# Optimization experiments

Hardware: AMD Instinct MI355X
Metric: run time of the kernel (lower is better)

## Reference

```python
import jax, jax.numpy as jnp
import numpy as np

N_ENT = 50000
N_REL = 16
N_EDGE = 1000000
D = 64


def setup_inputs() -> dict:
    key = jax.random.key(0)
    ks = jax.random.split(key, 20)
    inp = {
        'ent_embed': jax.random.normal(ks[0], (N_ENT, D), jnp.float32) * 0.1,
        'rel_embed': jax.random.normal(ks[1], (N_REL, D), jnp.float32) * 0.1,
        'W_R': jax.random.normal(ks[2], (N_REL, D, D), jnp.float32) * 0.1,
        'W1_0': jax.random.normal(ks[3], (64, 64), jnp.float32) * 0.1,
        'b1_0': jax.random.normal(ks[4], (64,), jnp.float32) * 0.1,
        'W2_0': jax.random.normal(ks[5], (64, 64), jnp.float32) * 0.1,
        'b2_0': jax.random.normal(ks[6], (64,), jnp.float32) * 0.1,
        'W1_1': jax.random.normal(ks[7], (64, 32), jnp.float32) * 0.1,
        'b1_1': jax.random.normal(ks[8], (32,), jnp.float32) * 0.1,
        'W2_1': jax.random.normal(ks[9], (64, 32), jnp.float32) * 0.1,
        'b2_1': jax.random.normal(ks[10], (32,), jnp.float32) * 0.1,
        'W1_2': jax.random.normal(ks[11], (32, 16), jnp.float32) * 0.1,
        'b1_2': jax.random.normal(ks[12], (16,), jnp.float32) * 0.1,
        'W2_2': jax.random.normal(ks[13], (32, 16), jnp.float32) * 0.1,
        'b2_2': jax.random.normal(ks[14], (16,), jnp.float32) * 0.1,
        'src': jax.random.randint(ks[15], (N_EDGE,), 0, N_ENT, jnp.int32),
        'dst': jax.random.randint(ks[16], (N_EDGE,), 0, N_ENT, jnp.int32),
        'etype': jax.random.randint(ks[17], (N_EDGE,), 0, N_REL, jnp.int32),
    }
    return inp


def _l2_normalize(x, eps=1e-12):
    # matches torch F.normalize(p=2, dim=1)
    n = jnp.sqrt(jnp.sum(x * x, axis=1, keepdims=True))
    return x / jnp.maximum(n, eps)


def _kgat_forward(ent_embed, rel_embed, W_R, layer_params, src, dst, etype):
    N = ent_embed.shape[0]
    # --- compute_attention: per-relation TransR projection of all entities ---
    # equivalent to per-edge ent[src] @ W_R[type] without materializing [E, D, D]
    proj = jnp.einsum('nd,rde->rne', ent_embed, W_R)          # [R, N, D]
    r_mul_t = proj[etype, src]                                # [E, D] (tail = src)
    r_mul_h = proj[etype, dst]                                # [E, D] (head = dst)
    att = jnp.sum(r_mul_t * jnp.tanh(r_mul_h + rel_embed[etype]), axis=-1)  # [E]
    # edge softmax grouped by destination node
    m = jax.ops.segment_max(att, dst, num_segments=N)         # [N]
    e = jnp.exp(att - m[dst])
    s = jax.ops.segment_sum(e, dst, num_segments=N)           # [N]
    a = e / s[dst]                                            # [E]

    # --- cf_embedding: bi-interaction aggregator layers ---
    h = ent_embed
    all_embed = [h]
    for (W1, b1, W2, b2) in layer_params:
        msg = a[:, None] * h[src]                             # [E, d_in]
        N_h = jax.ops.segment_sum(msg, dst, num_segments=N)   # [N, d_in]
        out = (jax.nn.leaky_relu((h + N_h) @ W1 + b1, 0.01)
               + jax.nn.leaky_relu((h * N_h) @ W2 + b2, 0.01))
        h = out
        all_embed.append(_l2_normalize(out))
    return jnp.concatenate(all_embed, axis=1)                 # [N, 64+64+32+16=176]


def reference(ent_embed, rel_embed, W_R,
              W1_0, b1_0, W2_0, b2_0,
              W1_1, b1_1, W2_1, b2_1,
              W1_2, b1_2, W2_2, b2_2,
              src, dst, etype):
    layer_params = [(W1_0, b1_0, W2_0, b2_0),
                    (W1_1, b1_1, W2_1, b2_1),
                    (W1_2, b1_2, W2_2, b2_2)]
    return _kgat_forward(ent_embed, rel_embed, W_R, layer_params, src, dst, etype)
```

## Files before the change

kernel.cpp:

```cpp
#include <hip/hip_runtime.h>
#include <hip/hip_bf16.h>
#include <cmath>

#define N_ENT  50000
#define N_RELS 16
#define N_EDGE 1000000
#define DIM    64
#define OUT_STRIDE 176

typedef float f32x4 __attribute__((ext_vector_type(4)));
typedef short s16x8 __attribute__((ext_vector_type(8)));

__device__ inline void bf16x8_unpack(uint4 u, float* f) {
    f[0] = __uint_as_float((u.x & 0xffffu) << 16);
    f[1] = __uint_as_float(u.x & 0xffff0000u);
    f[2] = __uint_as_float((u.y & 0xffffu) << 16);
    f[3] = __uint_as_float(u.y & 0xffff0000u);
    f[4] = __uint_as_float((u.z & 0xffffu) << 16);
    f[5] = __uint_as_float(u.z & 0xffff0000u);
    f[6] = __uint_as_float((u.w & 0xffffu) << 16);
    f[7] = __uint_as_float(u.w & 0xffff0000u);
}

__device__ inline ushort f2bf(float x) {
    __hip_bfloat16 b = __float2bfloat16(x);
    return *(ushort*)&b;
}

__device__ inline uint cvt_pk_bf16(float lo, float hi) {
    uint r;
    asm("v_cvt_pk_bf16_f32 %0, %1, %2" : "=v"(r) : "v"(lo), "v"(hi));
    return r;
}

__device__ __host__ inline int pcol(int p) {
    int qp = (p >> 3) & 7;
    int k  = p & 7;
    return 16 * (k >> 1) + 2 * qp + (k & 1);
}

__global__ __launch_bounds__(256) void prep_convert_kernel(
        const float* __restrict__ ent,
        ushort* __restrict__ ent_pi,
        float* __restrict__ out) {
    int i = blockIdx.x * blockDim.x + threadIdx.x;
    if (i < N_ENT * DIM) {
        float v = ent[i];
        ushort b = f2bf(v);
        int n = i >> 6, c = i & 63;
        int pos = ((c & 15) >> 1) * 8 + ((c >> 4) << 1) + (c & 1);
        ent_pi[(size_t)n * 64 + pos] = b;
        out[(size_t)n * OUT_STRIDE + c] = v;
    }
}

__global__ __launch_bounds__(256) void scan1_kernel(
        const int* __restrict__ counts, int* __restrict__ excl,
        int* __restrict__ bsum, int n) {
    __shared__ int sh[256];
    int t = threadIdx.x;
    int i = blockIdx.x * 256 + t;
    int c = (i < n) ? counts[i] : 0;
    sh[t] = c;
    __syncthreads();
    for (int off = 1; off < 256; off <<= 1) {
        int v = (t >= off) ? sh[t - off] : 0;
        __syncthreads();
        sh[t] += v;
        __syncthreads();
    }
    if (i < n) excl[i] = sh[t] - c;
    if (t == 255) bsum[blockIdx.x] = sh[255];
}

__global__ __launch_bounds__(256) void scan2_kernel(
        const int* __restrict__ bsum, int* __restrict__ boff,
        int* __restrict__ row_ptr, int nb, int n) {
    __shared__ int sh[256];
    int t = threadIdx.x;
    int v = (t < nb) ? bsum[t] : 0;
    sh[t] = v;
    __syncthreads();
    for (int off = 1; off < 256; off <<= 1) {
        int x = (t >= off) ? sh[t - off] : 0;
        __syncthreads();
        sh[t] += x;
        __syncthreads();
    }
    if (t < nb) boff[t] = sh[t] - v;
    if (t == nb - 1) row_ptr[n] = sh[t];
}

__global__ __launch_bounds__(256) void scan3_pos_kernel(
        const int* __restrict__ excl, const int* __restrict__ boff,
        int* __restrict__ row_ptr,
        const int* __restrict__ src, const int* __restrict__ dst,
        const int* __restrict__ etype, const int* __restrict__ off,
        unsigned long long* __restrict__ einfo) {
    int i = blockIdx.x * blockDim.x + threadIdx.x;
    if (i < N_ENT) row_ptr[i] = excl[i] + boff[i >> 8];
    if (i < N_EDGE) {
        int d = dst[i];
        int pos = excl[d] + boff[d >> 8] + off[i];
        unsigned long long info =
              (unsigned long long)(unsigned)src[i]
            | ((unsigned long long)(unsigned)d << 16)
            | ((unsigned long long)(unsigned)etype[i] << 32);
        einfo[pos] = info;
    }
}

__device__ __forceinline__ void gz_body(
        int r, int wid, int nw, int lane,
        const ushort* __restrict__ ent_pi,
        const float*  __restrict__ W_R,
        const float*  __restrict__ rel,
        ushort* __restrict__ Z,
        float* __restrict__ myLds) {
    int m = lane & 15;
    int q = lane >> 4;

    const float* Wr = W_R + (size_t)r * DIM * DIM;
    s16x8 b1[4][2], b2[4][2];
#pragma unroll
    for (int c = 0; c < 4; ++c)
#pragma unroll
        for (int ch = 0; ch < 2; ++ch)
#pragma unroll
            for (int j = 0; j < 8; ++j) {
                b1[c][ch][j] = (short)f2bf(Wr[pcol(ch * 32 + q * 8 + j) * DIM + c * 16 + m]);
                b2[c][ch][j] = (short)f2bf(Wr[(c * 16 + m) * DIM + ch * 32 + q * 8 + j]);
            }
    float relv[4];
#pragma unroll
    for (int c = 0; c < 4; ++c) relv[c] = rel[r * DIM + c * 16 + m];

    int par = m & 1;
    const int ntiles = N_ENT / 16;

    for (int t = wid; t < ntiles; t += nw) {
        int row0 = t * 16;
        const s16x8* arow = (const s16x8*)(ent_pi + (size_t)(row0 + m) * DIM);
        s16x8 a0 = arow[q];
        s16x8 a1 = arow[4 + q];
        f32x4 acc[4];
#pragma unroll
        for (int c = 0; c < 4; ++c) acc[c] = (f32x4){0.f, 0.f, 0.f, 0.f};
#pragma unroll
        for (int c = 0; c < 4; ++c) {
            acc[c] = __builtin_amdgcn_mfma_f32_16x16x32_bf16(a0, b1[c][0], acc[c], 0, 0, 0);
            acc[c] = __builtin_amdgcn_mfma_f32_16x16x32_bf16(a1, b1[c][1], acc[c], 0, 0, 0);
        }
#pragma unroll
        for (int c = 0; c < 4; ++c)
#pragma unroll
            for (int i = 0; i < 4; ++i) {
                float x = acc[c][i] + relv[c];
                float e2 = __expf(2.f * x);
                float g = 1.f - 2.f * __builtin_amdgcn_rcpf(e2 + 1.f);
                myLds[(q * 4 + i) * 68 + c * 16 + m] = g;
            }
        union { uint u[4]; s16x8 v; } a2u[2];
#pragma unroll
        for (int ch = 0; ch < 2; ++ch) {
            const f32x4* gp = (const f32x4*)(myLds + m * 68 + ch * 32 + q * 8);
            f32x4 g0 = gp[0];
            f32x4 g1 = gp[1];
            a2u[ch].u[0] = cvt_pk_bf16(g0[0], g0[1]);
            a2u[ch].u[1] = cvt_pk_bf16(g0[2], g0[3]);
            a2u[ch].u[2] = cvt_pk_bf16(g1[0], g1[1]);
            a2u[ch].u[3] = cvt_pk_bf16(g1[2], g1[3]);
        }

        f32x4 zacc[4];
#pragma unroll
        for (int c = 0; c < 4; ++c) zacc[c] = (f32x4){0.f, 0.f, 0.f, 0.f};
#pragma unroll
        for (int c = 0; c < 4; ++c) {
            zacc[c] = __builtin_amdgcn_mfma_f32_16x16x32_bf16(a2u[0].v, b2[c][0], zacc[c], 0, 0, 0);
            zacc[c] = __builtin_amdgcn_mfma_f32_16x16x32_bf16(a2u[1].v, b2[c][1], zacc[c], 0, 0, 0);
        }

        int rowA = row0 + 4 * q + (par ? 2 : 0);
        ushort* zb = Z + ((size_t)r * N_ENT + rowA) * 64 + (m >> 1) * 8;
#pragma unroll
        for (int rep = 0; rep < 2; ++rep) {
            uint4 Wv;
#pragma unroll
            for (int c = 0; c < 4; ++c) {
                float send = par ? zacc[c][rep] : zacc[c][2 + rep];
                float own  = par ? zacc[c][2 + rep] : zacc[c][rep];
                float oth  = __shfl_xor(send, 1, 64);
                float lo = par ? oth : own;
                float hi = par ? own : oth;
                ((uint*)&Wv)[c] = cvt_pk_bf16(lo, hi);
            }
            *(uint4*)(zb + rep * 64) = Wv;
        }
    }
}

#define HIST_LANES 131072

__global__ __launch_bounds__(256, 4) void gz_hist_kernel(
        const ushort* __restrict__ ent_pi,
        const float*  __restrict__ W_R,
        const float*  __restrict__ rel,
        ushort* __restrict__ Z,
        const int* __restrict__ dst,
        int* __restrict__ counts,
        int* __restrict__ off) {
    __shared__ __align__(16) float lds[3][16 * 68 + 16];
    int lane = threadIdx.x & 63;
    int wv   = threadIdx.x >> 6;

    if (wv == 3) {
        int lane_gid = blockIdx.x * 64 + lane;
        int d[8]; bool v[8]; int o[8];
#pragma unroll
        for (int k = 0; k < 8; ++k) {
            int i = lane_gid + k * HIST_LANES;
            v[k] = (i < N_EDGE);
            d[k] = v[k] ? dst[i] : 0;
        }
#pragma unroll
        for (int k = 0; k < 8; ++k)
            if (v[k]) o[k] = atomicAdd(&counts[d[k]], 1);
#pragma unroll
        for (int k = 0; k < 8; ++k)
            if (v[k]) off[lane_gid + k * HIST_LANES] = o[k];
        return;
    }

    int r   = blockIdx.x >> 7;
    int xb  = blockIdx.x & 127;
    int wid = xb * 3 + wv;
    gz_body(r, wid, 384, lane, ent_pi, W_R, rel, Z, lds[wv]);
}

__global__ __launch_bounds__(256) void att_dot_kernel(
        const ushort* __restrict__ ent_pi,
        const ushort* __restrict__ Z,
        const unsigned long long* __restrict__ einfo,
        uint2* __restrict__ es_csr,
        int n_edge) {
    int tid  = blockIdx.x * blockDim.x + threadIdx.x;
    int lane = threadIdx.x & 63;
    int sub  = lane >> 3;
    int q    = lane & 7;
    int base = (tid >> 6) * 32;
    if (base >= n_edge) return;

    int e[4];
    unsigned long long inf[4];
#pragma unroll
    for (int k = 0; k < 4; ++k) {
        e[k] = base + k * 8 + sub;
        inf[k] = einfo[e[k]];
    }

    int s[4], p_r[4], p_d[4];
#pragma unroll
    for (int k = 0; k < 4; ++k) {
        s[k]   = (int)(inf[k] & 0xffffu);
        p_d[k] = (int)((inf[k] >> 16) & 0xffffu);
        p_r[k] = (int)((inf[k] >> 32) & 0xfu);
    }

    uint4 uz[4], ue[4];
#pragma unroll
    for (int k = 0; k < 4; ++k) {
        uz[k] = *(const uint4*)(Z + ((size_t)p_r[k] * N_ENT + p_d[k]) * DIM + q * 8);
        ue[k] = *(const uint4*)(ent_pi + (size_t)s[k] * DIM + q * 8);
    }

    float pr[4];
#pragma unroll
    for (int k = 0; k < 4; ++k) {
        float zv[8], ev[8];
        bf16x8_unpack(uz[k], zv);
        bf16x8_unpack(ue[k], ev);
        float p = 0.f;
#pragma unroll
        for (int j = 0; j < 8; ++j) p = fmaf(ev[j], zv[j], p);
        pr[k] = p;
    }
#pragma unroll
    for (int k = 0; k < 4; ++k) {
        pr[k] += __shfl_xor(pr[k], 1, 64);
        pr[k] += __shfl_xor(pr[k], 2, 64);
        pr[k] += __shfl_xor(pr[k], 4, 64);
    }

    if (q == 0) {
#pragma unroll
        for (int k = 0; k < 4; ++k)
            es_csr[e[k]] = make_uint2(__float_as_uint(pr[k]), (unsigned)s[k]);
    }
}

__global__ __launch_bounds__(256) void agg64s_kernel(
        const ushort* __restrict__ tab,
        const uint2* __restrict__ es_csr,
        const int* __restrict__ row_ptr,
        float2* __restrict__ stats,
        float* __restrict__ N_h, int n_node) {
    int wid  = (blockIdx.x * blockDim.x + threadIdx.x) >> 6;
    int lane = threadIdx.x & 63;
    if (wid >= n_node) return;
    int q   = lane & 7;
    int sub = lane >> 3;

    int start = row_ptr[wid], end = row_ptr[wid + 1];

    float mx = -INFINITY;
    for (int i = start + lane; i < end; i += 64)
        mx = fmaxf(mx, __uint_as_float(es_csr[i].x));
#pragma unroll
    for (int o = 32; o > 0; o >>= 1)
        mx = fmaxf(mx, __shfl_xor(mx, o, 64));
    float ssum = 0.f;
    for (int i = start + lane; i < end; i += 64)
        ssum += __expf(__uint_as_float(es_csr[i].x) - mx);
#pragma unroll
    for (int o = 32; o > 0; o >>= 1)
        ssum += __shfl_xor(ssum, o, 64);
    float inv = (end > start) ? (1.0f / ssum) : 0.f;
    if (lane == 0) stats[wid] = make_float2(mx, inv);

    float acc[8];
#pragma unroll
    for (int j = 0; j < 8; ++j) acc[j] = 0.f;

    for (int p = start + sub; p < end; p += 8) {
        uint2 es = es_csr[p];
        float av = __expf(__uint_as_float(es.x) - mx);
        int   si = (int)es.y;
        uint4 u  = *(const uint4*)(tab + (size_t)si * 64 + q * 8);
        float g[8];
        bf16x8_unpack(u, g);
#pragma unroll
        for (int j = 0; j < 8; ++j) acc[j] = fmaf(av, g[j], acc[j]);
    }
#pragma unroll
    for (int mask = 8; mask < 64; mask <<= 1)
#pragma unroll
        for (int j = 0; j < 8; ++j)
            acc[j] += __shfl_xor(acc[j], mask, 64);

    if (sub == 0) {
        float* dstp = N_h + (size_t)wid * 64 + q * 8;
        *(float4*)(dstp)     = (float4){acc[0] * inv, acc[1] * inv, acc[2] * inv, acc[3] * inv};
        *(float4*)(dstp + 4) = (float4){acc[4] * inv, acc[5] * inv, acc[6] * inv, acc[7] * inv};
    }
}

__global__ __launch_bounds__(256) void agg64_kernel(
        const ushort* __restrict__ tab,
        const uint2* __restrict__ es_csr,
        const int* __restrict__ row_ptr,
        const float2* __restrict__ stats,
        float* __restrict__ N_h, int n_node) {
    int wid  = (blockIdx.x * blockDim.x + threadIdx.x) >> 6;
    int lane = threadIdx.x & 63;
    if (wid >= n_node) return;
    int q   = lane & 7;
    int sub = lane >> 3;

    int start = row_ptr[wid], end = row_ptr[wid + 1];
    float2 st = stats[wid];
    float mx = st.x, inv = st.y;
    float acc[8];
#pragma unroll
    for (int j = 0; j < 8; ++j) acc[j] = 0.f;

    for (int p = start + sub; p < end; p += 8) {
        uint2 es = es_csr[p];
        float av = __expf(__uint_as_float(es.x) - mx);
        int   si = (int)es.y;
        uint4 u  = *(const uint4*)(tab + (size_t)si * 64 + q * 8);
        float g[8];
        bf16x8_unpack(u, g);
#pragma unroll
        for (int j = 0; j < 8; ++j) acc[j] = fmaf(av, g[j], acc[j]);
    }
#pragma unroll
    for (int mask = 8; mask < 64; mask <<= 1)
#pragma unroll
        for (int j = 0; j < 8; ++j)
            acc[j] += __shfl_xor(acc[j], mask, 64);

    if (sub == 0) {
        float* dstp = N_h + (size_t)wid * 64 + q * 8;
        *(float4*)(dstp)     = (float4){acc[0] * inv, acc[1] * inv, acc[2] * inv, acc[3] * inv};
        *(float4*)(dstp + 4) = (float4){acc[4] * inv, acc[5] * inv, acc[6] * inv, acc[7] * inv};
    }
}

__global__ __launch_bounds__(256) void agg32_kernel(
        const ushort* __restrict__ tab,
        const uint2* __restrict__ es_csr,
        const int* __restrict__ row_ptr,
        const float2* __restrict__ stats,
        float* __restrict__ N_h, int n_node) {
    int wid  = (blockIdx.x * blockDim.x + threadIdx.x) >> 6;
    int lane = threadIdx.x & 63;
    if (wid >= n_node) return;
    int q   = lane & 3;
    int sub = lane >> 2;

    int start = row_ptr[wid], end = row_ptr[wid + 1];
    float2 st = stats[wid];
    float mx = st.x, inv = st.y;
    float acc[8];
#pragma unroll
    for (int j = 0; j < 8; ++j) acc[j] = 0.f;

    for (int p = start + sub; p < end; p += 16) {
        uint2 es = es_csr[p];
        float av = __expf(__uint_as_float(es.x) - mx);
        int   si = (int)es.y;
        uint4 u  = *(const uint4*)(tab + (size_t)si * 32 + q * 8);
        float g[8];
        bf16x8_unpack(u, g);
#pragma unroll
        for (int j = 0; j < 8; ++j) acc[j] = fmaf(av, g[j], acc[j]);
    }
#pragma unroll
    for (int mask = 4; mask < 64; mask <<= 1)
#pragma unroll
        for (int j = 0; j < 8; ++j)
            acc[j] += __shfl_xor(acc[j], mask, 64);

    if (sub == 0) {
        float* dstp = N_h + (size_t)wid * 32 + q * 8;
        *(float4*)(dstp)     = (float4){acc[0] * inv, acc[1] * inv, acc[2] * inv, acc[3] * inv};
        *(float4*)(dstp + 4) = (float4){acc[4] * inv, acc[5] * inv, acc[6] * inv, acc[7] * inv};
    }
}

template <int D_IN, int D_OUT, bool PERM>
__global__ __launch_bounds__(256) void mlp_mfma_kernel(
        const ushort* __restrict__ h,
        const float* __restrict__ N_h,
        const float* __restrict__ W1, const float* __restrict__ b1,
        const float* __restrict__ W2, const float* __restrict__ b2,
        ushort* __restrict__ ho,
        float* __restrict__ out_buf, int out_col) {
    constexpr int CH = D_IN / 32;
    constexpr int CT = D_OUT / 16;

    int lane = threadIdx.x & 63;
    int m    = lane & 15;
    int q    = lane >> 4;
    int wid  = blockIdx.x * (blockDim.x >> 6) + (threadIdx.x >> 6);
    int nw   = gridDim.x * (blockDim.x >> 6);

    s16x8 bu[CT][CH], bv[CT][CH];
#pragma unroll
    for (int c = 0; c < CT; ++c)
#pragma unroll
        for (int ch = 0; ch < CH; ++ch)
#pragma unroll
            for (int j = 0; j < 8; ++j) {
                int p = ch * 32 + q * 8 + j;
                int k = PERM ? pcol(p) : p;
                bu[c][ch][j] = (short)f2bf(W1[k * D_OUT + c * 16 + m]);
                bv[c][ch][j] = (short)f2bf(W2[k * D_OUT + c * 16 + m]);
            }

    const int ntiles = N_ENT / 16;
    for (int t = wid; t < ntiles; t += nw) {
        int row0 = t * 16;
        s16x8 au[CH], av[CH];
#pragma unroll
        for (int ch = 0; ch < CH; ++ch) {
            uint4 hu = *(const uint4*)(h + (size_t)(row0 + m) * D_IN + ch * 32 + q * 8);
            float hv8[8];
            bf16x8_unpack(hu, hv8);
            const float4* np = (const float4*)(N_h + (size_t)(row0 + m) * D_IN + ch * 32 + q * 8);
            float4 na = np[0], nb = np[1];
            float nv[8] = {na.x, na.y, na.z, na.w, nb.x, nb.y, nb.z, nb.w};
#pragma unroll
            for (int j = 0; j < 8; ++j) {
                au[ch][j] = (short)f2bf(hv8[j] + nv[j]);
                av[ch][j] = (short)f2bf(hv8[j] * nv[j]);
            }
        }

        f32x4 accu[CT], accv[CT];
#pragma unroll
        for (int c = 0; c < CT; ++c) {
            accu[c] = (f32x4){0.f, 0.f, 0.f, 0.f};
            accv[c] = (f32x4){0.f, 0.f, 0.f, 0.f};
        }
#pragma unroll
        for (int c = 0; c < CT; ++c)
#pragma unroll
            for (int ch = 0; ch < CH; ++ch) {
                accu[c] = __builtin_amdgcn_mfma_f32_16x16x32_bf16(au[ch], bu[c][ch], accu[c], 0, 0, 0);
                accv[c] = __builtin_amdgcn_mfma_f32_16x16x32_bf16(av[ch], bv[c][ch], accv[c], 0, 0, 0);
            }

        float res[CT][4];
        float sq[4] = {0.f, 0.f, 0.f, 0.f};
#pragma unroll
        for (int c = 0; c < CT; ++c) {
            float bb1 = b1[c * 16 + m];
            float bb2 = b2[c * 16 + m];
#pragma unroll
            for (int i = 0; i < 4; ++i) {
                float o1 = accu[c][i] + bb1;
                float o2 = accv[c][i] + bb2;
                float r1 = (o1 >= 0.f) ? o1 : 0.01f * o1;
                float r2 = (o2 >= 0.f) ? o2 : 0.01f * o2;
                float rr = r1 + r2;
                res[c][i] = rr;
                sq[i] = fmaf(rr, rr, sq[i]);
            }
        }
#pragma unroll
        for (int mask = 1; mask < 16; mask <<= 1)
#pragma unroll
            for (int i = 0; i < 4; ++i)
                sq[i] += __shfl_xor(sq[i], mask, 64);

#pragma unroll
        for (int i = 0; i < 4; ++i) {
            int row = row0 + q * 4 + i;
            float inv = 1.f / fmaxf(sqrtf(sq[i]), 1e-12f);
#pragma unroll
            for (int c = 0; c < CT; ++c) {
                int col = c * 16 + m;
                out_buf[(size_t)row * OUT_STRIDE + out_col + col] = res[c][i] * inv;
                if (ho) ho[(size_t)row * D_OUT + col] = f2bf(res[c][i]);
            }
        }
    }
}

extern "C" void kernel_launch(void* const* d_in, const int* in_sizes, int n_in,
                              void* d_out, int out_size, void* d_ws, size_t ws_size,
                              hipStream_t stream) {
    const float* ent  = (const float*)d_in[0];
    const float* rel  = (const float*)d_in[1];
    const float* W_R  = (const float*)d_in[2];
    const float* W1_0 = (const float*)d_in[3];
    const float* b1_0 = (const float*)d_in[4];
    const float* W2_0 = (const float*)d_in[5];
    const float* b2_0 = (const float*)d_in[6];
    const float* W1_1 = (const float*)d_in[7];
    const float* b1_1 = (const float*)d_in[8];
    const float* W2_1 = (const float*)d_in[9];
    const float* b2_1 = (const float*)d_in[10];
    const float* W1_2 = (const float*)d_in[11];
    const float* b1_2 = (const float*)d_in[12];
    const float* W2_2 = (const float*)d_in[13];
    const float* b2_2 = (const float*)d_in[14];
    const int*   src   = (const int*)d_in[15];
    const int*   dst   = (const int*)d_in[16];
    const int*   etype = (const int*)d_in[17];
    float* out = (float*)d_out;

    char* w = (char*)d_ws;
    uint2*  es_csr  = (uint2*)w;  w += (size_t)N_EDGE * 8;
    int*    counts  = (int*)w;    w += (size_t)(N_ENT + 64) * 4;
    int*    row_ptr = (int*)w;    w += (size_t)(N_ENT + 64) * 4;
    float2* stats   = (float2*)w; w += (size_t)(N_ENT + 64) * 8;
    int*    excl    = (int*)w;    w += (size_t)(N_ENT + 64) * 4;
    int*    bsum    = (int*)w;    w += 256 * 4;
    int*    boff    = (int*)w;    w += 256 * 4;
    ushort* ent_pi  = (ushort*)w; w += (size_t)N_ENT * 64 * 2;
    ushort* h1      = (ushort*)w; w += (size_t)N_ENT * 64 * 2;
    ushort* h2      = (ushort*)w; w += (size_t)N_ENT * 32 * 2;
    float*  N_h     = (float*)w;  w += (size_t)N_ENT * 64 * 4;
    ushort* Z       = (ushort*)w;
    (void)ws_size;

    int* off = (int*)es_csr;
    unsigned long long* einfo = (unsigned long long*)N_h;

    hipMemsetAsync(counts, 0, (size_t)N_ENT * 4, stream);

    const int nb = (N_ENT + 255) / 256;

    prep_convert_kernel<<<(N_ENT * DIM + 255) / 256, 256, 0, stream>>>(
        ent, ent_pi, out);

    gz_hist_kernel<<<2048, 256, 0, stream>>>(
        ent_pi, W_R, rel, Z, dst, counts, off);

    scan1_kernel<<<nb, 256, 0, stream>>>(counts, excl, bsum, N_ENT);
    scan2_kernel<<<1, 256, 0, stream>>>(bsum, boff, row_ptr, nb, N_ENT);
    scan3_pos_kernel<<<(N_EDGE + 255) / 256, 256, 0, stream>>>(
        excl, boff, row_ptr, src, dst, etype, off, einfo);

    att_dot_kernel<<<((N_EDGE + 31) / 32 * 64 + 255) / 256, 256, 0, stream>>>(
        ent_pi, Z, einfo, es_csr, N_EDGE);

    const int aggGrid = (N_ENT + 3) / 4;
    const int mlpGrid = 782;

    agg64s_kernel<<<aggGrid, 256, 0, stream>>>(ent_pi, es_csr, row_ptr, stats, N_h, N_ENT);
    mlp_mfma_kernel<64, 64, true><<<mlpGrid, 256, 0, stream>>>(
        ent_pi, N_h, W1_0, b1_0, W2_0, b2_0, h1, out, 64);

    agg64_kernel<<<aggGrid, 256, 0, stream>>>(h1, es_csr, row_ptr, stats, N_h, N_ENT);
    mlp_mfma_kernel<64, 32, false><<<mlpGrid, 256, 0, stream>>>(
        h1, N_h, W1_1, b1_1, W2_1, b2_1, h2, out, 128);

    agg32_kernel<<<aggGrid, 256, 0, stream>>>(h2, es_csr, row_ptr, stats, N_h, N_ENT);
    mlp_mfma_kernel<32, 16, false><<<mlpGrid, 256, 0, stream>>>(
        h2, N_h, W1_2, b1_2, W2_2, b2_2, nullptr, out, 160);
}
```

Baseline: 363.4 us.

## Rebalance gz/histogram wave split and double edges per wave in att_dot

The gz_hist kernel now gives the histogram role to only half the blocks, with each histogram wave handling 16 edges per lane instead of 8. The freed waves join the Z projection, raising the number of gz workers from 384 to 448 per relation. The att_dot kernel now processes 64 edges per wave, with 8 outstanding gather loads per lane and bounds checks on each edge, aiming for more memory-level parallelism. The trade-off is more register pressure and longer atomic chains on the histogram waves.

```diff
diff --git a/kernel.cpp b/kernel.cpp
--- a/kernel.cpp
+++ b/kernel.cpp
@@ -200,7 +200,7 @@
     }
 }
 
-#define HIST_LANES 131072
+#define HIST_LANES 65536
 
 __global__ __launch_bounds__(256, 4) void gz_hist_kernel(
         const ushort* __restrict__ ent_pi,
@@ -210,32 +210,35 @@
         const int* __restrict__ dst,
         int* __restrict__ counts,
         int* __restrict__ off) {
-    __shared__ __align__(16) float lds[3][16 * 68 + 16];
+    __shared__ __align__(16) float lds[4][16 * 68 + 16];
     int lane = threadIdx.x & 63;
     int wv   = threadIdx.x >> 6;
-
-    if (wv == 3) {
-        int lane_gid = blockIdx.x * 64 + lane;
-        int d[8]; bool v[8]; int o[8];
-#pragma unroll
-        for (int k = 0; k < 8; ++k) {
-            int i = lane_gid + k * HIST_LANES;
-            v[k] = (i < N_EDGE);
-            d[k] = v[k] ? dst[i] : 0;
-        }
-#pragma unroll
-        for (int k = 0; k < 8; ++k)
-            if (v[k]) o[k] = atomicAdd(&counts[d[k]], 1);
-#pragma unroll
-        for (int k = 0; k < 8; ++k)
-            if (v[k]) off[lane_gid + k * HIST_LANES] = o[k];
+    int xb   = blockIdx.x & 127;
+
+    if ((xb & 1) && wv == 3) {
+        int lane_gid = (blockIdx.x >> 1) * 64 + lane;
+#pragma unroll
+        for (int half = 0; half < 2; ++half) {
+            int d[8]; bool v[8]; int o[8];
+#pragma unroll
+            for (int k = 0; k < 8; ++k) {
+                int i = lane_gid + (half * 8 + k) * HIST_LANES;
+                v[k] = (i < N_EDGE);
+                d[k] = v[k] ? dst[i] : 0;
+            }
+#pragma unroll
+            for (int k = 0; k < 8; ++k)
+                if (v[k]) o[k] = atomicAdd(&counts[d[k]], 1);
+#pragma unroll
+            for (int k = 0; k < 8; ++k)
+                if (v[k]) off[lane_gid + (half * 8 + k) * HIST_LANES] = o[k];
+        }
         return;
     }
 
     int r   = blockIdx.x >> 7;
-    int xb  = blockIdx.x & 127;
-    int wid = xb * 3 + wv;
-    gz_body(r, wid, 384, lane, ent_pi, W_R, rel, Z, lds[wv]);
+    int g   = xb * 4 - (xb >> 1) + wv;
+    gz_body(r, g, 448, lane, ent_pi, W_R, rel, Z, lds[wv]);
 }
 
 __global__ __launch_bounds__(256) void att_dot_kernel(
@@ -248,35 +251,30 @@
     int lane = threadIdx.x & 63;
     int sub  = lane >> 3;
     int q    = lane & 7;
-    int base = (tid >> 6) * 32;
+    int base = (tid >> 6) * 64;
     if (base >= n_edge) return;
 
-    int e[4];
-    unsigned long long inf[4];
-#pragma unroll
-    for (int k = 0; k < 4; ++k) {
+    int e[8];
+    unsigned long long inf[8];
+#pragma unroll
+    for (int k = 0; k < 8; ++k) {
         e[k] = base + k * 8 + sub;
-        inf[k] = einfo[e[k]];
-    }
-
-    int s[4], p_r[4], p_d[4];
-#pragma unroll
-    for (int k = 0; k < 4; ++k) {
-        s[k]   = (int)(inf[k] & 0xffffu);
-        p_d[k] = (int)((inf[k] >> 16) & 0xffffu);
-        p_r[k] = (int)((inf[k] >> 32) & 0xfu);
-    }
-
-    uint4 uz[4], ue[4];
-#pragma unroll
-    for (int k = 0; k < 4; ++k) {
-        uz[k] = *(const uint4*)(Z + ((size_t)p_r[k] * N_ENT + p_d[k]) * DIM + q * 8);
-        ue[k] = *(const uint4*)(ent_pi + (size_t)s[k] * DIM + q * 8);
-    }
-
-    float pr[4];
-#pragma unroll
-    for (int k = 0; k < 4; ++k) {
+        inf[k] = (e[k] < n_edge) ? einfo[e[k]] : 0ull;
+    }
+
+    uint4 uz[8], ue[8];
+#pragma unroll
+    for (int k = 0; k < 8; ++k) {
+        int s = (int)(inf[k] & 0xffffu);
+        int d = (int)((inf[k] >> 16) & 0xffffu);
+        int r = (int)((inf[k] >> 32) & 0xfu);
+        uz[k] = *(const uint4*)(Z + ((size_t)r * N_ENT + d) * DIM + q * 8);
+        ue[k] = *(const uint4*)(ent_pi + (size_t)s * DIM + q * 8);
+    }
+
+    float pr[8];
+#pragma unroll
+    for (int k = 0; k < 8; ++k) {
         float zv[8], ev[8];
         bf16x8_unpack(uz[k], zv);
         bf16x8_unpack(ue[k], ev);
@@ -286,7 +284,7 @@
         pr[k] = p;
     }
 #pragma unroll
-    for (int k = 0; k < 4; ++k) {
+    for (int k = 0; k < 8; ++k) {
         pr[k] += __shfl_xor(pr[k], 1, 64);
         pr[k] += __shfl_xor(pr[k], 2, 64);
         pr[k] += __shfl_xor(pr[k], 4, 64);
@@ -294,8 +292,10 @@
 
     if (q == 0) {
 #pragma unroll
-        for (int k = 0; k < 4; ++k)
-            es_csr[e[k]] = make_uint2(__float_as_uint(pr[k]), (unsigned)s[k]);
+        for (int k = 0; k < 8; ++k)
+            if (e[k] < n_edge)
+                es_csr[e[k]] = make_uint2(__float_as_uint(pr[k]),
+                                          (unsigned)(inf[k] & 0xffffu));
     }
 }
 
@@ -595,7 +595,7 @@
     scan3_pos_kernel<<<(N_EDGE + 255) / 256, 256, 0, stream>>>(
         excl, boff, row_ptr, src, dst, etype, off, einfo);
 
-    att_dot_kernel<<<((N_EDGE + 31) / 32 * 64 + 255) / 256, 256, 0, stream>>>(
+    att_dot_kernel<<<((N_EDGE + 63) / 64 * 64 + 255) / 256, 256, 0, stream>>>(
         ent_pi, Z, einfo, es_csr, N_EDGE);
 
     const int aggGrid = (N_ENT + 3) / 4;
```

New measurement: 376.3 us. 1.04x slower.
